# Kernel optimization log

Hardware: AMD Instinct MI355X
Metric: run time of the kernel (lower is better)

The kernel has to match this reference:

```python
import jax, jax.numpy as jnp
import numpy as np

D = 128      # state_dim
ED = 20      # edge_dim (RBF basis size)
R = 3        # num message/update rounds
G = 3        # gated equivariant blocks
CUT = 5.0    # cutoff
N = 10000    # nodes
E = 160000   # edges
B = 500      # molecules
HRO = 64     # readout hidden


def setup_inputs() -> dict:
    key = jax.random.key(0)
    ks = jax.random.split(key, 40)
    sc = 0.05

    def nrm(k, shape):
        return jax.random.normal(k, shape, dtype=jnp.float32) * sc

    inp = {
        "h": jax.random.normal(ks[0], (N, 5), dtype=jnp.float32),
        "pos": jax.random.normal(ks[1], (N, 3), dtype=jnp.float32),
        "edge_index": jax.random.randint(ks[2], (2, E), 0, N),
        "batch": jnp.sort(jax.random.randint(ks[3], (N,), 0, B)),
        # node embedding Linear(5, D)
        "emb_w": nrm(ks[4], (5, D)), "emb_b": nrm(ks[5], (D,)),
        # per-round message params (stacked over rounds)
        "msg_phi_w1": nrm(ks[6], (R, D, D)), "msg_phi_b1": nrm(ks[7], (R, D)),
        "msg_phi_w2": nrm(ks[8], (R, D, 3 * D)), "msg_phi_b2": nrm(ks[9], (R, 3 * D)),
        "msg_filt_w": nrm(ks[10], (R, ED, 3 * D)), "msg_filt_b": nrm(ks[11], (R, 3 * D)),
        # per-round update params
        "upd_U": nrm(ks[12], (R, D, D)), "upd_V": nrm(ks[13], (R, D, D)),
        "upd_w1": nrm(ks[14], (R, 2 * D, D)), "upd_b1": nrm(ks[15], (R, D)),
        "upd_w2": nrm(ks[16], (R, D, 3 * D)), "upd_b2": nrm(ks[17], (R, 3 * D)),
        # gated equivariant blocks
        "geb_wv1": nrm(ks[18], (G, D, D)), "geb_wv2": nrm(ks[19], (G, D, D)),
        "geb_w1": nrm(ks[20], (G, 2 * D, D)), "geb_b1": nrm(ks[21], (G, D)),
        "geb_w2": nrm(ks[22], (G, D, 2 * D)), "geb_b2": nrm(ks[23], (G, 2 * D)),
        # invariant readout MLP
        "ro_w1": nrm(ks[24], (D, HRO)), "ro_b1": nrm(ks[25], (HRO,)),
        "ro_w2": nrm(ks[26], (HRO, 1)), "ro_b2": nrm(ks[27], (1,)),
    }
    return inp


def _safe_norm(x, axis):
    return jnp.sqrt(jnp.sum(x * x, axis=axis) + 1e-8)


def reference(h, pos, edge_index, batch,
              emb_w, emb_b,
              msg_phi_w1, msg_phi_b1, msg_phi_w2, msg_phi_b2,
              msg_filt_w, msg_filt_b,
              upd_U, upd_V, upd_w1, upd_b1, upd_w2, upd_b2,
              geb_wv1, geb_wv2, geb_w1, geb_b1, geb_w2, geb_b2,
              ro_w1, ro_b1, ro_w2, ro_b2):
    n_nodes = h.shape[0]
    row, col = edge_index[0], edge_index[1]
    # edge vectors: r_ij = pos[col] - pos[row]
    r_ij = pos[col] - pos[row]                                   # [E,3]
    d = jnp.clip(jnp.linalg.norm(r_ij, axis=1, keepdims=True), 1e-6, None)  # [E,1]
    unit = r_ij / d                                              # [E,3]
    # sinc radial basis + cosine cutoff
    freqs = jnp.arange(1, ED + 1, dtype=h.dtype)
    rbf = jnp.sin(freqs * jnp.pi * d / CUT) / d                  # [E,ED]
    fcut = 0.5 * (jnp.cos(jnp.pi * d / CUT) + 1.0) * (d < CUT)   # [E,1]

    s = h @ emb_w + emb_b                                        # [N,D]
    v = jnp.zeros((n_nodes, D, 3), dtype=h.dtype)                # [N,D,3]

    for r in range(R):
        # --- PaiNNMessage ---
        phi = jax.nn.silu(s @ msg_phi_w1[r] + msg_phi_b1[r]) @ msg_phi_w2[r] + msg_phi_b2[r]  # [N,3D]
        filt = (rbf @ msg_filt_w[r] + msg_filt_b[r]) * fcut      # [E,3D]
        x = phi[col] * filt                                      # gather + modulate  [E,3D]
        xs, xvv, xvw = jnp.split(x, 3, axis=-1)                  # each [E,D]
        ds = jax.ops.segment_sum(xs, row, num_segments=n_nodes)  # [N,D]
        dv_e = xvv[:, :, None] * v[col] + xvw[:, :, None] * unit[:, None, :]  # [E,D,3]
        dv = jax.ops.segment_sum(dv_e, row, num_segments=n_nodes)             # [N,D,3]
        s = s + ds
        v = v + dv
        # --- PaiNNUpdate ---
        Uv = jnp.einsum('ndc,de->nec', v, upd_U[r])              # [N,D,3]
        Vv = jnp.einsum('ndc,de->nec', v, upd_V[r])              # [N,D,3]
        Vn = _safe_norm(Vv, axis=-1)                             # [N,D]
        a = jax.nn.silu(jnp.concatenate([s, Vn], axis=-1) @ upd_w1[r] + upd_b1[r]) @ upd_w2[r] + upd_b2[r]
        a_ss, a_sv, a_vv = jnp.split(a, 3, axis=-1)
        s = s + a_ss + a_sv * jnp.sum(Uv * Vv, axis=-1)
        v = v + a_vv[:, :, None] * Uv

    # --- GatedEquivariantBlocks ---
    for g in range(G):
        v1 = jnp.einsum('ndc,de->nec', v, geb_wv1[g])
        v2 = jnp.einsum('ndc,de->nec', v, geb_wv2[g])
        n2 = _safe_norm(v2, axis=-1)                             # [N,D]
        a = jax.nn.silu(jnp.concatenate([s, n2], axis=-1) @ geb_w1[g] + geb_b1[g]) @ geb_w2[g] + geb_b2[g]
        s_new, gate = jnp.split(a, 2, axis=-1)
        s = s_new
        v = gate[:, :, None] * v1

    # --- InvariantReadout + molwise scatter ---
    out = jax.nn.silu(s @ ro_w1 + ro_b1) @ ro_w2 + ro_b2         # [N,1]
    molwise = jax.ops.segment_sum(out, batch, num_segments=B)    # [B,1]
    return molwise.squeeze(-1)
```

## Files before the change

### kernel.cpp

```cpp
#include <hip/hip_runtime.h>

typedef __attribute__((ext_vector_type(4))) float f32x4;
typedef __attribute__((ext_vector_type(8))) short short8;

#define D 128
#define D3 384
#define SLD 256
#define EDIM 20
#define NR 3
#define NG 3
#define CUTOFF 5.0f
#define NNODES 10000
#define NEDGES 160000
#define NMOL 500
#define HROH 64
#define PI_F 3.14159265358979323846f

#define FBIAS 1
#define FSILU 2
#define FBF16O 4

static __device__ __forceinline__ float silu_f(float x) {
    return x / (1.0f + expf(-x));
}

static __device__ __forceinline__ ushort f2bf(float x) {
    uint u = __float_as_uint(x);
    uint r = (u + 0x7fffu + ((u >> 16) & 1u)) >> 16;
    return (ushort)r;
}
static __device__ __forceinline__ float bf2f(ushort h) {
    return __uint_as_float((uint)h << 16);
}

#define TLR 64
#define TLC 64
#define KC 32
#define APAD 40
#define BPAD 36

__global__ __launch_bounds__(256) void gemm_k(
    const float* __restrict__ A, int lda,
    const float* __restrict__ W, int ldw,
    const float* __restrict__ bias,
    float* __restrict__ C, ushort* __restrict__ Cbf, int ldc,
    int N, int K, int flags)
{
    const int n0 = blockIdx.x * TLR;
    const int m0 = blockIdx.y * TLC;
    __shared__ ushort Ah[TLR * APAD], Al[TLR * APAD];
    __shared__ ushort Bh[TLC * BPAD], Bl[TLC * BPAD];
    const int tid = threadIdx.x;
    const int arow = tid & 63;
    const int akq = (tid >> 6) * 4;
    const bool aok = (n0 + arow) < N;
    const float* Ar = A + (size_t)(n0 + arow) * lda;
    const int bk = tid >> 4;
    const int bm = (tid & 15) * 4;
    const float* Wp = W + m0 + bm;
    const int lane = tid & 63;
    const int wrow = (tid >> 6) * 16;
    const int fr = lane & 15;
    const int kg = lane >> 4;
    const ushort* aph = Ah + (wrow + fr) * APAD + kg * 8;
    const ushort* apl = Al + (wrow + fr) * APAD + kg * 8;

    f32x4 acc[4];
    #pragma unroll
    for (int t = 0; t < 4; ++t) acc[t] = (f32x4){0.f, 0.f, 0.f, 0.f};

    for (int k0 = 0; k0 < K; k0 += KC) {
        #pragma unroll
        for (int half = 0; half < 2; ++half) {
            int kk = akq + half * 16;
            float4 v = aok ? *(const float4*)(Ar + k0 + kk)
                           : make_float4(0.f, 0.f, 0.f, 0.f);
            ushort h0 = f2bf(v.x), h1 = f2bf(v.y), h2 = f2bf(v.z), h3 = f2bf(v.w);
            ushort l0 = f2bf(v.x - bf2f(h0)), l1 = f2bf(v.y - bf2f(h1));
            ushort l2 = f2bf(v.z - bf2f(h2)), l3 = f2bf(v.w - bf2f(h3));
            uint2 ph, pl;
            ph.x = (uint)h0 | ((uint)h1 << 16); ph.y = (uint)h2 | ((uint)h3 << 16);
            pl.x = (uint)l0 | ((uint)l1 << 16); pl.y = (uint)l2 | ((uint)l3 << 16);
            *(uint2*)(Ah + arow * APAD + kk) = ph;
            *(uint2*)(Al + arow * APAD + kk) = pl;
        }
        #pragma unroll
        for (int half = 0; half < 2; ++half) {
            int kk = bk + half * 16;
            float4 v = *(const float4*)(Wp + (size_t)(k0 + kk) * ldw);
            float vv[4] = {v.x, v.y, v.z, v.w};
            #pragma unroll
            for (int i = 0; i < 4; ++i) {
                ushort hh = f2bf(vv[i]);
                ushort ll = f2bf(vv[i] - bf2f(hh));
                Bh[(bm + i) * BPAD + kk] = hh;
                Bl[(bm + i) * BPAD + kk] = ll;
            }
        }
        __syncthreads();
        short8 ah = *(const short8*)aph;
        short8 al = *(const short8*)apl;
        #pragma unroll
        for (int t = 0; t < 4; ++t) {
            const ushort* bp = Bh + (t * 16 + fr) * BPAD + kg * 8;
            const ushort* bq = Bl + (t * 16 + fr) * BPAD + kg * 8;
            short8 bh, bl;
            ((uint2*)&bh)[0] = *(const uint2*)bp;
            ((uint2*)&bh)[1] = *(const uint2*)(bp + 4);
            ((uint2*)&bl)[0] = *(const uint2*)bq;
            ((uint2*)&bl)[1] = *(const uint2*)(bq + 4);
            acc[t] = __builtin_amdgcn_mfma_f32_16x16x32_bf16(ah, bh, acc[t], 0, 0, 0);
            acc[t] = __builtin_amdgcn_mfma_f32_16x16x32_bf16(al, bh, acc[t], 0, 0, 0);
            acc[t] = __builtin_amdgcn_mfma_f32_16x16x32_bf16(ah, bl, acc[t], 0, 0, 0);
        }
        __syncthreads();
    }
    #pragma unroll
    for (int t = 0; t < 4; ++t) {
        #pragma unroll
        for (int r = 0; r < 4; ++r) {
            int n = n0 + wrow + kg * 4 + r;
            if (n < N) {
                int m = m0 + t * 16 + fr;
                float val = acc[t][r];
                if (flags & FBIAS) val += bias[m];
                if (flags & FSILU) val = silu_f(val);
                if (flags & FBF16O) Cbf[(size_t)n * ldc + m] = f2bf(val);
                else                C[(size_t)n * ldc + m] = val;
            }
        }
    }
}

template <bool WITHDOT>
__global__ __launch_bounds__(256) void uvn_k(
    const float* __restrict__ A,
    const float* __restrict__ WU, const float* __restrict__ WV,
    float* __restrict__ Uv,
    float* __restrict__ DOT,
    float* __restrict__ SX, int N)
{
    const int n0 = blockIdx.x * 64;
    const int m0 = blockIdx.y * 64;
    __shared__ ushort Ah[3][64 * APAD], Al[3][64 * APAD];
    __shared__ ushort Bh[2][64 * BPAD], Bl[2][64 * BPAD];
    const int tid = threadIdx.x;
    const int arow = tid & 63;
    const int akq = (tid >> 6) * 4;
    const bool aok = (n0 + arow) < N;
    const float* Ar = A + (size_t)(n0 + arow) * D3;
    const int bk = tid >> 4;
    const int bm = (tid & 15) * 4;
    const int lane = tid & 63;
    const int wrow = (tid >> 6) * 16;
    const int fr = lane & 15;
    const int kg = lane >> 4;

    f32x4 acc[3][2][4];
    #pragma unroll
    for (int c = 0; c < 3; ++c)
        #pragma unroll
        for (int s = 0; s < 2; ++s)
            #pragma unroll
            for (int t = 0; t < 4; ++t) acc[c][s][t] = (f32x4){0.f, 0.f, 0.f, 0.f};

    for (int k0 = 0; k0 < D; k0 += KC) {
        #pragma unroll
        for (int c = 0; c < 3; ++c) {
            #pragma unroll
            for (int half = 0; half < 2; ++half) {
                int kk = akq + half * 16;
                float4 v = aok ? *(const float4*)(Ar + c * D + k0 + kk)
                               : make_float4(0.f, 0.f, 0.f, 0.f);
                ushort h0 = f2bf(v.x), h1 = f2bf(v.y), h2 = f2bf(v.z), h3 = f2bf(v.w);
                ushort l0 = f2bf(v.x - bf2f(h0)), l1 = f2bf(v.y - bf2f(h1));
                ushort l2 = f2bf(v.z - bf2f(h2)), l3 = f2bf(v.w - bf2f(h3));
                uint2 ph, pl;
                ph.x = (uint)h0 | ((uint)h1 << 16); ph.y = (uint)h2 | ((uint)h3 << 16);
                pl.x = (uint)l0 | ((uint)l1 << 16); pl.y = (uint)l2 | ((uint)l3 << 16);
                *(uint2*)(&Ah[c][arow * APAD + kk]) = ph;
                *(uint2*)(&Al[c][arow * APAD + kk]) = pl;
            }
        }
        #pragma unroll
        for (int s = 0; s < 2; ++s) {
            const float* W = s ? WV : WU;
            #pragma unroll
            for (int half = 0; half < 2; ++half) {
                int kk = bk + half * 16;
                float4 v = *(const float4*)(W + (size_t)(k0 + kk) * D + m0 + bm);
                float vv[4] = {v.x, v.y, v.z, v.w};
                #pragma unroll
                for (int i = 0; i < 4; ++i) {
                    ushort hh = f2bf(vv[i]);
                    ushort ll = f2bf(vv[i] - bf2f(hh));
                    Bh[s][(bm + i) * BPAD + kk] = hh;
                    Bl[s][(bm + i) * BPAD + kk] = ll;
                }
            }
        }
        __syncthreads();
        short8 ah[3], al[3];
        #pragma unroll
        for (int c = 0; c < 3; ++c) {
            ah[c] = *(const short8*)(&Ah[c][(wrow + fr) * APAD + kg * 8]);
            al[c] = *(const short8*)(&Al[c][(wrow + fr) * APAD + kg * 8]);
        }
        #pragma unroll
        for (int t = 0; t < 4; ++t) {
            #pragma unroll
            for (int s = 0; s < 2; ++s) {
                const ushort* bp = &Bh[s][(t * 16 + fr) * BPAD + kg * 8];
                const ushort* bq = &Bl[s][(t * 16 + fr) * BPAD + kg * 8];
                short8 bh, bl;
                ((uint2*)&bh)[0] = *(const uint2*)bp;
                ((uint2*)&bh)[1] = *(const uint2*)(bp + 4);
                ((uint2*)&bl)[0] = *(const uint2*)bq;
                ((uint2*)&bl)[1] = *(const uint2*)(bq + 4);
                #pragma unroll
                for (int c = 0; c < 3; ++c) {
                    acc[c][s][t] = __builtin_amdgcn_mfma_f32_16x16x32_bf16(ah[c], bh, acc[c][s][t], 0, 0, 0);
                    acc[c][s][t] = __builtin_amdgcn_mfma_f32_16x16x32_bf16(al[c], bh, acc[c][s][t], 0, 0, 0);
                    acc[c][s][t] = __builtin_amdgcn_mfma_f32_16x16x32_bf16(ah[c], bl, acc[c][s][t], 0, 0, 0);
                }
            }
        }
        __syncthreads();
    }
    #pragma unroll
    for (int t = 0; t < 4; ++t) {
        #pragma unroll
        for (int r = 0; r < 4; ++r) {
            int n = n0 + wrow + kg * 4 + r;
            if (n < N) {
                int m = m0 + t * 16 + fr;
                float ux = acc[0][0][t][r], uy = acc[1][0][t][r], uz = acc[2][0][t][r];
                float vx = acc[0][1][t][r], vy = acc[1][1][t][r], vz = acc[2][1][t][r];
                float* up = Uv + (size_t)n * D3 + m;
                up[0]     = ux;
                up[D]     = uy;
                up[2 * D] = uz;
                SX[(size_t)n * SLD + D + m] =
                    sqrtf(fmaf(vx, vx, fmaf(vy, vy, fmaf(vz, vz, 1e-8f))));
                if (WITHDOT)
                    DOT[(size_t)n * D + m] = fmaf(ux, vx, fmaf(uy, vy, uz * vz));
            }
        }
    }
}

__global__ __launch_bounds__(256) void emb_k(
    const float* __restrict__ h, const float* __restrict__ w,
    const float* __restrict__ b, float* __restrict__ s, int total)
{
    int i = blockIdx.x * 256 + threadIdx.x;
    if (i >= total) return;
    int n = i >> 7, d = i & 127;
    float acc = b[d];
    #pragma unroll
    for (int k = 0; k < 5; ++k) acc = fmaf(h[n * 5 + k], w[k * D + d], acc);
    s[(size_t)n * SLD + d] = acc;
}

__global__ __launch_bounds__(256) void hist_k(const int* __restrict__ ei,
                                              int* __restrict__ cnt, int E)
{
    int e = blockIdx.x * 256 + threadIdx.x;
    if (e < E) atomicAdd(&cnt[ei[e]], 1);
}

__global__ __launch_bounds__(256) void scan_k(const int* __restrict__ cnt,
                                              int* __restrict__ offs, int n)
{
    __shared__ int tmp[256];
    __shared__ int carry;
    if (threadIdx.x == 0) carry = 0;
    __syncthreads();
    for (int base = 0; base < n; base += 256) {
        int i = base + threadIdx.x;
        int v = (i < n) ? cnt[i] : 0;
        tmp[threadIdx.x] = v;
        __syncthreads();
        for (int off = 1; off < 256; off <<= 1) {
            int add = (threadIdx.x >= off) ? tmp[threadIdx.x - off] : 0;
            __syncthreads();
            tmp[threadIdx.x] += add;
            __syncthreads();
        }
        if (i < n) offs[i + 1] = carry + tmp[threadIdx.x];
        __syncthreads();
        if (threadIdx.x == 255) carry += tmp[255];
        __syncthreads();
    }
    if (threadIdx.x == 0) offs[0] = 0;
}

__global__ __launch_bounds__(256) void initnext_k(const int* __restrict__ offs,
                                                  int* __restrict__ next, int n)
{
    int i = blockIdx.x * 256 + threadIdx.x;
    if (i < n) next[i] = offs[i];
}

__global__ __launch_bounds__(256) void edge_pre_k(
    const int* __restrict__ ei, const float* __restrict__ pos,
    int* __restrict__ next, float* __restrict__ rbf_s,
    float* __restrict__ uf_s, int* __restrict__ col_s, int E)
{
    int e = blockIdx.x * 256 + threadIdx.x;
    if (e >= E) return;
    int r = ei[e], c = ei[E + e];
    float dx = pos[c * 3 + 0] - pos[r * 3 + 0];
    float dy = pos[c * 3 + 1] - pos[r * 3 + 1];
    float dz = pos[c * 3 + 2] - pos[r * 3 + 2];
    float dist = sqrtf(dx * dx + dy * dy + dz * dz);
    float d = fmaxf(dist, 1e-6f);
    float inv = 1.0f / d;
    int p = atomicAdd(&next[r], 1);
    col_s[p] = c;
    uf_s[p * 4 + 0] = dx * inv;
    uf_s[p * 4 + 1] = dy * inv;
    uf_s[p * 4 + 2] = dz * inv;
    uf_s[p * 4 + 3] = (d < CUTOFF) ? 0.5f * (cosf(PI_F * d / CUTOFF) + 1.0f) : 0.0f;
    float w = PI_F * d / CUTOFF;
    #pragma unroll
    for (int k = 1; k <= EDIM; ++k)
        rbf_s[(size_t)p * EDIM + (k - 1)] = sinf((float)k * w) * inv;
}

#define MSG_NPB 4
__global__ __launch_bounds__(256) void message_csr_k(
    const int* __restrict__ offs, const int* __restrict__ col_s,
    const float* __restrict__ rbf_s, const float* __restrict__ uf_s,
    const ushort* __restrict__ Pbf, const float* __restrict__ Vold,
    const ushort* __restrict__ VbfOld,
    const float* __restrict__ Wf, const float* __restrict__ bf,
    float* __restrict__ S, float* __restrict__ Vnew,
    ushort* __restrict__ VbfNew, int N)
{
    const int sub = threadIdx.x >> 7;
    const int d = threadIdx.x & 127;
    float ws[EDIM], wvv[EDIM], wvw[EDIM];
    #pragma unroll
    for (int k = 0; k < EDIM; ++k) {
        ws[k]  = Wf[k * D3 + d];
        wvv[k] = Wf[k * D3 + D + d];
        wvw[k] = Wf[k * D3 + 2 * D + d];
    }
    const float bs = bf[d], bvv = bf[D + d], bvw = bf[2 * D + d];

    auto edge = [&](int j, float& ds, float& dvx, float& dvy, float& dvz) {
        float4 u4 = *(const float4*)(uf_s + (size_t)j * 4);
        int col = col_s[j];
        const float* rb = rbf_s + (size_t)j * EDIM;
        float4 r0 = *(const float4*)(rb);
        float4 r1 = *(const float4*)(rb + 4);
        float4 r2 = *(const float4*)(rb + 8);
        float4 r3 = *(const float4*)(rb + 12);
        float4 r4 = *(const float4*)(rb + 16);
        float rv[EDIM] = {r0.x, r0.y, r0.z, r0.w, r1.x, r1.y, r1.z, r1.w,
                          r2.x, r2.y, r2.z, r2.w, r3.x, r3.y, r3.z, r3.w,
                          r4.x, r4.y, r4.z, r4.w};
        float fs = bs, fvv = bvv, fvw = bvw;
        #pragma unroll
        for (int k = 0; k < EDIM; ++k) {
            fs  = fmaf(rv[k], ws[k], fs);
            fvv = fmaf(rv[k], wvv[k], fvv);
            fvw = fmaf(rv[k], wvw[k], fvw);
        }
        float fc = u4.w;
        const ushort* pc = Pbf + (size_t)col * D3;
        const ushort* vc = VbfOld + (size_t)col * D3;
        float xs  = bf2f(pc[d]) * fs * fc;
        float xvv = bf2f(pc[D + d]) * fvv * fc;
        float xvw = bf2f(pc[2 * D + d]) * fvw * fc;
        ds += xs;
        dvx = fmaf(xvv, bf2f(vc[d]),         fmaf(xvw, u4.x, dvx));
        dvy = fmaf(xvv, bf2f(vc[D + d]),     fmaf(xvw, u4.y, dvy));
        dvz = fmaf(xvv, bf2f(vc[2 * D + d]), fmaf(xvw, u4.z, dvz));
    };

    for (int it = 0; it < MSG_NPB / 2; ++it) {
        int n = blockIdx.x * MSG_NPB + it * 2 + sub;
        if (n >= N) return;
        float ds0 = 0.f, dx0 = 0.f, dy0 = 0.f, dz0 = 0.f;
        float ds1 = 0.f, dx1 = 0.f, dy1 = 0.f, dz1 = 0.f;
        const int j0 = offs[n], j1 = offs[n + 1];
        int j = j0;
        for (; j + 2 <= j1; j += 2) {
            edge(j, ds0, dx0, dy0, dz0);
            edge(j + 1, ds1, dx1, dy1, dz1);
        }
        if (j < j1) edge(j, ds0, dx0, dy0, dz0);
        S[(size_t)n * SLD + d] += ds0 + ds1;
        const float* vo = Vold + (size_t)n * D3;
        float* vn = Vnew + (size_t)n * D3;
        ushort* vb = VbfNew + (size_t)n * D3;
        float nx = vo[d] + dx0 + dx1;
        float ny = vo[D + d] + dy0 + dy1;
        float nz = vo[2 * D + d] + dz0 + dz1;
        vn[d] = nx;         vb[d] = f2bf(nx);
        vn[D + d] = ny;     vb[D + d] = f2bf(ny);
        vn[2 * D + d] = nz; vb[2 * D + d] = f2bf(nz);
    }
}

__global__ __launch_bounds__(256) void upd_apply_k(
    const float* __restrict__ U3, const float* __restrict__ DOT,
    const float* __restrict__ P, float* __restrict__ s,
    float* __restrict__ v, ushort* __restrict__ vbf, int total)
{
    int i = blockIdx.x * 256 + threadIdx.x;
    if (i >= total) return;
    int n = i >> 7, d = i & 127;
    const float* u = U3 + (size_t)n * D3;
    float ux = u[d], uy = u[D + d], uz = u[2 * D + d];
    const float* a = P + (size_t)n * D3;
    s[(size_t)n * SLD + d] += a[d] + a[D + d] * DOT[i];
    float avv = a[2 * D + d];
    float* vv = v + (size_t)n * D3;
    ushort* vb = vbf + (size_t)n * D3;
    float nx = fmaf(avv, ux, vv[d]);
    float ny = fmaf(avv, uy, vv[D + d]);
    float nz = fmaf(avv, uz, vv[2 * D + d]);
    vv[d] = nx;         vb[d] = f2bf(nx);
    vv[D + d] = ny;     vb[D + d] = f2bf(ny);
    vv[2 * D + d] = nz; vb[2 * D + d] = f2bf(nz);
}

__global__ __launch_bounds__(256) void geb_apply_k(
    const float* __restrict__ P, const float* __restrict__ U3,
    float* __restrict__ s, float* __restrict__ v, int total)
{
    int i = blockIdx.x * 256 + threadIdx.x;
    if (i >= total) return;
    int n = i >> 7, d = i & 127;
    const float* a = P + (size_t)n * 2 * D;
    s[(size_t)n * SLD + d] = a[d];
    float g = a[D + d];
    const float* u = U3 + (size_t)n * D3;
    float* vv = v + (size_t)n * D3;
    vv[d]         = g * u[d];
    vv[D + d]     = g * u[D + d];
    vv[2 * D + d] = g * u[2 * D + d];
}

__global__ __launch_bounds__(256) void readout_k(
    const float* __restrict__ H2, const float* __restrict__ w2,
    const float* __restrict__ b2, const int* __restrict__ batch,
    float* __restrict__ out, int N)
{
    int n = blockIdx.x * 256 + threadIdx.x;
    if (n >= N) return;
    float acc = b2[0];
    const float* hrow = H2 + (size_t)n * HROH;
    #pragma unroll
    for (int k = 0; k < HROH; ++k) acc = fmaf(hrow[k], w2[k], acc);
    atomicAdd(out + batch[n], acc);
}


static inline void gemm(hipStream_t st, const float* A, int lda,
                        const float* W, int ldw, const float* bias,
                        float* C, ushort* Cbf, int ldc,
                        int N, int K, int M, int flags)
{
    dim3 g((N + TLR - 1) / TLR, M / TLC, 1);
    hipLaunchKernelGGL(gemm_k, g, dim3(256), 0, st,
                       A, lda, W, ldw, bias, C, Cbf, ldc, N, K, flags);
}

extern "C" void kernel_launch(void* const* d_in, const int* in_sizes, int n_in,
                              void* d_out, int out_size, void* d_ws, size_t ws_size,
                              hipStream_t stream)
{
    const float* h          = (const float*)d_in[0];
    const float* pos        = (const float*)d_in[1];
    const int*   ei         = (const int*)d_in[2];
    const int*   batch      = (const int*)d_in[3];
    const float* emb_w      = (const float*)d_in[4];
    const float* emb_b      = (const float*)d_in[5];
    const float* msg_phi_w1 = (const float*)d_in[6];
    const float* msg_phi_b1 = (const float*)d_in[7];
    const float* msg_phi_w2 = (const float*)d_in[8];
    const float* msg_phi_b2 = (const float*)d_in[9];
    const float* msg_filt_w = (const float*)d_in[10];
    const float* msg_filt_b = (const float*)d_in[11];
    const float* upd_U      = (const float*)d_in[12];
    const float* upd_V      = (const float*)d_in[13];
    const float* upd_w1     = (const float*)d_in[14];
    const float* upd_b1     = (const float*)d_in[15];
    const float* upd_w2     = (const float*)d_in[16];
    const float* upd_b2     = (const float*)d_in[17];
    const float* geb_wv1    = (const float*)d_in[18];
    const float* geb_wv2    = (const float*)d_in[19];
    const float* geb_w1     = (const float*)d_in[20];
    const float* geb_b1     = (const float*)d_in[21];
    const float* geb_w2     = (const float*)d_in[22];
    const float* geb_b2     = (const float*)d_in[23];
    const float* ro_w1      = (const float*)d_in[24];
    const float* ro_b1      = (const float*)d_in[25];
    const float* ro_w2      = (const float*)d_in[26];
    const float* ro_b2      = (const float*)d_in[27];
    float* out = (float*)d_out;

    const int N = NNODES, E = NEDGES;

    char* p = (char*)d_ws;
    auto carve = [&](size_t bytes) {
        char* r = p;
        p += (bytes + 255) & ~(size_t)255;
        return r;
    };
    float*  SX   = (float*)carve((size_t)N * SLD * 4);
    float*  VA   = (float*)carve((size_t)N * D3 * 4);
    float*  VB   = (float*)carve((size_t)N * D3 * 4);
    float*  P_   = (float*)carve((size_t)N * D3 * 4);
    ushort* Pbf  = (ushort*)P_;
    ushort* VBFa = (ushort*)carve((size_t)N * D3 * 2);
    ushort* VBFb = (ushort*)carve((size_t)N * D3 * 2);
    float*  H    = (float*)carve((size_t)N * D * 4);
    float*  H2   = (float*)carve((size_t)N * D * 4);
    float*  RBFs = (float*)carve((size_t)E * EDIM * 4);
    float*  UFs  = (float*)carve((size_t)E * 4 * 4);
    int*    COLs = (int*)carve((size_t)E * 4);
    int*    offs = (int*)carve((size_t)(N + 1) * 4);
    int*    nxt  = (int*)carve((size_t)N * 4);

    hipMemsetAsync(VA, 0, (size_t)N * D3 * 4, stream);
    hipMemsetAsync(VBFa, 0, (size_t)N * D3 * 2, stream);
    hipLaunchKernelGGL(emb_k, dim3((N * D + 255) / 256), dim3(256), 0, stream,
                       h, emb_w, emb_b, SX, N * D);
    hipMemsetAsync(nxt, 0, (size_t)N * 4, stream);
    hipLaunchKernelGGL(hist_k, dim3((E + 255) / 256), dim3(256), 0, stream, ei, nxt, E);
    hipLaunchKernelGGL(scan_k, dim3(1), dim3(256), 0, stream, nxt, offs, N);
    hipLaunchKernelGGL(initnext_k, dim3((N + 255) / 256), dim3(256), 0, stream,
                       offs, nxt, N);
    hipLaunchKernelGGL(edge_pre_k, dim3((E + 255) / 256), dim3(256), 0, stream,
                       ei, pos, nxt, RBFs, UFs, COLs, E);

    float*  Vc = VA;   ushort* VbfC = VBFa;
    float*  Vs = VB;   ushort* VbfS = VBFb;

    for (int r = 0; r < NR; ++r) {
        gemm(stream, SX, SLD, msg_phi_w1 + (size_t)r * D * D, D,
             msg_phi_b1 + (size_t)r * D, H, nullptr, D, N, D, D, FBIAS | FSILU);
        gemm(stream, H, D, msg_phi_w2 + (size_t)r * D * D3, D3,
             msg_phi_b2 + (size_t)r * D3, nullptr, Pbf, D3, N, D, D3,
             FBIAS | FBF16O);
        hipLaunchKernelGGL(message_csr_k, dim3((N + MSG_NPB - 1) / MSG_NPB),
                           dim3(256), 0, stream,
                           offs, COLs, RBFs, UFs, Pbf, Vc, VbfC,
                           msg_filt_w + (size_t)r * EDIM * D3,
                           msg_filt_b + (size_t)r * D3, SX, Vs, VbfS, N);
        { float* t = Vc; Vc = Vs; Vs = t; }
        { ushort* t = VbfC; VbfC = VbfS; VbfS = t; }
        float* Uv = Vs;
        hipLaunchKernelGGL(HIP_KERNEL_NAME(uvn_k<true>),
                           dim3((N + 63) / 64, 2), dim3(256), 0, stream,
                           Vc, upd_U + (size_t)r * D * D,
                           upd_V + (size_t)r * D * D, Uv, H, SX, N);
        gemm(stream, SX, SLD, upd_w1 + (size_t)r * 2 * D * D, D,
             upd_b1 + (size_t)r * D, H2, nullptr, D, N, 2 * D, D, FBIAS | FSILU);
        gemm(stream, H2, D, upd_w2 + (size_t)r * D * D3, D3,
             upd_b2 + (size_t)r * D3, P_, nullptr, D3, N, D, D3, FBIAS);
        hipLaunchKernelGGL(upd_apply_k, dim3((N * D + 255) / 256), dim3(256), 0,
                           stream, Uv, H, P_, SX, Vc, VbfC, N * D);
    }

    for (int g = 0; g < NG; ++g) {
        float* Uv = Vs;
        hipLaunchKernelGGL(HIP_KERNEL_NAME(uvn_k<false>),
                           dim3((N + 63) / 64, 2), dim3(256), 0, stream,
                           Vc, geb_wv1 + (size_t)g * D * D,
                           geb_wv2 + (size_t)g * D * D, Uv, nullptr, SX, N);
        gemm(stream, SX, SLD, geb_w1 + (size_t)g * 2 * D * D, D,
             geb_b1 + (size_t)g * D, H2, nullptr, D, N, 2 * D, D, FBIAS | FSILU);
        gemm(stream, H2, D, geb_w2 + (size_t)g * D * 2 * D, 2 * D,
             geb_b2 + (size_t)g * 2 * D, P_, nullptr, 2 * D, N, D, 2 * D, FBIAS);
        hipLaunchKernelGGL(geb_apply_k, dim3((N * D + 255) / 256), dim3(256), 0,
                           stream, P_, Uv, SX, Vc, N * D);
    }

    gemm(stream, SX, SLD, ro_w1, HROH, ro_b1, H2, nullptr, HROH, N, D, HROH,
         FBIAS | FSILU);
    hipMemsetAsync(out, 0, (size_t)NMOL * 4, stream);
    hipLaunchKernelGGL(readout_k, dim3((N + 255) / 256), dim3(256), 0, stream,
                       H2, ro_w2, ro_b2, batch, out, N);
}
```

Before: 936.4 us.

## Precompute edge filters with MFMA GEMM and shrink uvn tile rows

The per-edge RBF filter projection (20x384 FMAs per edge, done inline in the message kernel with weights held in registers) is moved into a separate padded-K GEMM on the MFMA path. The cutoff factor is fused into the GEMM epilogue and the result is stored as bf16 per edge, so the message kernel only loads three bf16 filter values per edge. This adds a write and read of an E x 384 bf16 buffer each round and lowers filter precision to bf16. Separately, uvn_k is retiled to 32 rows per block with waves split over column halves, doubling the grid size.

```diff
diff --git a/kernel.cpp b/kernel.cpp
--- a/kernel.cpp
+++ b/kernel.cpp
@@ -7,6 +7,7 @@
 #define D3 384
 #define SLD 256
 #define EDIM 20
+#define KPAD 32
 #define NR 3
 #define NG 3
 #define CUTOFF 5.0f
@@ -19,6 +20,7 @@
 #define FBIAS 1
 #define FSILU 2
 #define FBF16O 4
+#define FFCUT 8
 
 static __device__ __forceinline__ float silu_f(float x) {
     return x / (1.0f + expf(-x));
@@ -42,7 +44,7 @@
 __global__ __launch_bounds__(256) void gemm_k(
     const float* __restrict__ A, int lda,
     const float* __restrict__ W, int ldw,
-    const float* __restrict__ bias,
+    const float* __restrict__ bias, const float* __restrict__ fcut,
     float* __restrict__ C, ushort* __restrict__ Cbf, int ldc,
     int N, int K, int flags)
 {
@@ -124,6 +126,7 @@
                 int m = m0 + t * 16 + fr;
                 float val = acc[t][r];
                 if (flags & FBIAS) val += bias[m];
+                if (flags & FFCUT) val *= fcut[(size_t)n * 4];
                 if (flags & FSILU) val = silu_f(val);
                 if (flags & FBF16O) Cbf[(size_t)n * ldc + m] = f2bf(val);
                 else                C[(size_t)n * ldc + m] = val;
@@ -140,47 +143,45 @@
     float* __restrict__ DOT,
     float* __restrict__ SX, int N)
 {
-    const int n0 = blockIdx.x * 64;
+    const int n0 = blockIdx.x * 32;
     const int m0 = blockIdx.y * 64;
-    __shared__ ushort Ah[3][64 * APAD], Al[3][64 * APAD];
+    __shared__ ushort Ah[3][32 * APAD], Al[3][32 * APAD];
     __shared__ ushort Bh[2][64 * BPAD], Bl[2][64 * BPAD];
     const int tid = threadIdx.x;
-    const int arow = tid & 63;
-    const int akq = (tid >> 6) * 4;
+    const int arow = tid & 31;
+    const int akq = (tid >> 5) * 4;
     const bool aok = (n0 + arow) < N;
     const float* Ar = A + (size_t)(n0 + arow) * D3;
     const int bk = tid >> 4;
     const int bm = (tid & 15) * 4;
+    const int w = tid >> 6;
+    const int rt = w & 1;
+    const int ch = w >> 1;
     const int lane = tid & 63;
-    const int wrow = (tid >> 6) * 16;
     const int fr = lane & 15;
     const int kg = lane >> 4;
 
-    f32x4 acc[3][2][4];
+    f32x4 acc[3][2][2];
     #pragma unroll
     for (int c = 0; c < 3; ++c)
         #pragma unroll
         for (int s = 0; s < 2; ++s)
             #pragma unroll
-            for (int t = 0; t < 4; ++t) acc[c][s][t] = (f32x4){0.f, 0.f, 0.f, 0.f};
+            for (int t = 0; t < 2; ++t) acc[c][s][t] = (f32x4){0.f, 0.f, 0.f, 0.f};
 
     for (int k0 = 0; k0 < D; k0 += KC) {
         #pragma unroll
         for (int c = 0; c < 3; ++c) {
-            #pragma unroll
-            for (int half = 0; half < 2; ++half) {
-                int kk = akq + half * 16;
-                float4 v = aok ? *(const float4*)(Ar + c * D + k0 + kk)
-                               : make_float4(0.f, 0.f, 0.f, 0.f);
-                ushort h0 = f2bf(v.x), h1 = f2bf(v.y), h2 = f2bf(v.z), h3 = f2bf(v.w);
-                ushort l0 = f2bf(v.x - bf2f(h0)), l1 = f2bf(v.y - bf2f(h1));
-                ushort l2 = f2bf(v.z - bf2f(h2)), l3 = f2bf(v.w - bf2f(h3));
-                uint2 ph, pl;
-                ph.x = (uint)h0 | ((uint)h1 << 16); ph.y = (uint)h2 | ((uint)h3 << 16);
-                pl.x = (uint)l0 | ((uint)l1 << 16); pl.y = (uint)l2 | ((uint)l3 << 16);
-                *(uint2*)(&Ah[c][arow * APAD + kk]) = ph;
-                *(uint2*)(&Al[c][arow * APAD + kk]) = pl;
-            }
+            float4 v = aok ? *(const float4*)(Ar + c * D + k0 + akq)
+                           : make_float4(0.f, 0.f, 0.f, 0.f);
+            ushort h0 = f2bf(v.x), h1 = f2bf(v.y), h2 = f2bf(v.z), h3 = f2bf(v.w);
+            ushort l0 = f2bf(v.x - bf2f(h0)), l1 = f2bf(v.y - bf2f(h1));
+            ushort l2 = f2bf(v.z - bf2f(h2)), l3 = f2bf(v.w - bf2f(h3));
+            uint2 ph, pl;
+            ph.x = (uint)h0 | ((uint)h1 << 16); ph.y = (uint)h2 | ((uint)h3 << 16);
+            pl.x = (uint)l0 | ((uint)l1 << 16); pl.y = (uint)l2 | ((uint)l3 << 16);
+            *(uint2*)(&Ah[c][arow * APAD + akq]) = ph;
+            *(uint2*)(&Al[c][arow * APAD + akq]) = pl;
         }
         #pragma unroll
         for (int s = 0; s < 2; ++s) {
@@ -203,15 +204,15 @@
         short8 ah[3], al[3];
         #pragma unroll
         for (int c = 0; c < 3; ++c) {
-            ah[c] = *(const short8*)(&Ah[c][(wrow + fr) * APAD + kg * 8]);
-            al[c] = *(const short8*)(&Al[c][(wrow + fr) * APAD + kg * 8]);
-        }
-        #pragma unroll
-        for (int t = 0; t < 4; ++t) {
+            ah[c] = *(const short8*)(&Ah[c][(rt * 16 + fr) * APAD + kg * 8]);
+            al[c] = *(const short8*)(&Al[c][(rt * 16 + fr) * APAD + kg * 8]);
+        }
+        #pragma unroll
+        for (int t = 0; t < 2; ++t) {
             #pragma unroll
             for (int s = 0; s < 2; ++s) {
-                const ushort* bp = &Bh[s][(t * 16 + fr) * BPAD + kg * 8];
-                const ushort* bq = &Bl[s][(t * 16 + fr) * BPAD + kg * 8];
+                const ushort* bp = &Bh[s][(ch * 32 + t * 16 + fr) * BPAD + kg * 8];
+                const ushort* bq = &Bl[s][(ch * 32 + t * 16 + fr) * BPAD + kg * 8];
                 short8 bh, bl;
                 ((uint2*)&bh)[0] = *(const uint2*)bp;
                 ((uint2*)&bh)[1] = *(const uint2*)(bp + 4);
@@ -228,12 +229,12 @@
         __syncthreads();
     }
     #pragma unroll
-    for (int t = 0; t < 4; ++t) {
+    for (int t = 0; t < 2; ++t) {
         #pragma unroll
         for (int r = 0; r < 4; ++r) {
-            int n = n0 + wrow + kg * 4 + r;
+            int n = n0 + rt * 16 + kg * 4 + r;
             if (n < N) {
-                int m = m0 + t * 16 + fr;
+                int m = m0 + ch * 32 + t * 16 + fr;
                 float ux = acc[0][0][t][r], uy = acc[1][0][t][r], uz = acc[2][0][t][r];
                 float vx = acc[0][1][t][r], vy = acc[1][1][t][r], vz = acc[2][1][t][r];
                 float* up = Uv + (size_t)n * D3 + m;
@@ -260,6 +261,17 @@
     #pragma unroll
     for (int k = 0; k < 5; ++k) acc = fmaf(h[n * 5 + k], w[k * D + d], acc);
     s[(size_t)n * SLD + d] = acc;
+}
+
+__global__ __launch_bounds__(256) void wfpad_k(const float* __restrict__ w,
+                                               float* __restrict__ wp)
+{
+    int i = blockIdx.x * 256 + threadIdx.x;
+    if (i >= 3 * KPAD * D3) return;
+    int r = i / (KPAD * D3);
+    int rem = i % (KPAD * D3);
+    int k = rem / D3, m = rem % D3;
+    wp[i] = (k < EDIM) ? w[((size_t)r * EDIM + k) * D3 + m] : 0.f;
 }
 
 __global__ __launch_bounds__(256) void hist_k(const int* __restrict__ ei,
@@ -323,57 +335,38 @@
     uf_s[p * 4 + 2] = dz * inv;
     uf_s[p * 4 + 3] = (d < CUTOFF) ? 0.5f * (cosf(PI_F * d / CUTOFF) + 1.0f) : 0.0f;
     float w = PI_F * d / CUTOFF;
+    float* rb = rbf_s + (size_t)p * KPAD;
     #pragma unroll
     for (int k = 1; k <= EDIM; ++k)
-        rbf_s[(size_t)p * EDIM + (k - 1)] = sinf((float)k * w) * inv;
+        rb[k - 1] = sinf((float)k * w) * inv;
+    #pragma unroll
+    for (int k = EDIM; k < KPAD; ++k) rb[k] = 0.f;
 }
 
 #define MSG_NPB 4
 __global__ __launch_bounds__(256) void message_csr_k(
     const int* __restrict__ offs, const int* __restrict__ col_s,
-    const float* __restrict__ rbf_s, const float* __restrict__ uf_s,
+    const ushort* __restrict__ FILT, const float* __restrict__ uf_s,
     const ushort* __restrict__ Pbf, const float* __restrict__ Vold,
     const ushort* __restrict__ VbfOld,
-    const float* __restrict__ Wf, const float* __restrict__ bf,
     float* __restrict__ S, float* __restrict__ Vnew,
     ushort* __restrict__ VbfNew, int N)
 {
     const int sub = threadIdx.x >> 7;
     const int d = threadIdx.x & 127;
-    float ws[EDIM], wvv[EDIM], wvw[EDIM];
-    #pragma unroll
-    for (int k = 0; k < EDIM; ++k) {
-        ws[k]  = Wf[k * D3 + d];
-        wvv[k] = Wf[k * D3 + D + d];
-        wvw[k] = Wf[k * D3 + 2 * D + d];
-    }
-    const float bs = bf[d], bvv = bf[D + d], bvw = bf[2 * D + d];
 
     auto edge = [&](int j, float& ds, float& dvx, float& dvy, float& dvz) {
+        const ushort* fp = FILT + (size_t)j * D3;
+        float f0 = bf2f(fp[d]);
+        float f1 = bf2f(fp[D + d]);
+        float f2 = bf2f(fp[2 * D + d]);
+        int col = col_s[j];
         float4 u4 = *(const float4*)(uf_s + (size_t)j * 4);
-        int col = col_s[j];
-        const float* rb = rbf_s + (size_t)j * EDIM;
-        float4 r0 = *(const float4*)(rb);
-        float4 r1 = *(const float4*)(rb + 4);
-        float4 r2 = *(const float4*)(rb + 8);
-        float4 r3 = *(const float4*)(rb + 12);
-        float4 r4 = *(const float4*)(rb + 16);
-        float rv[EDIM] = {r0.x, r0.y, r0.z, r0.w, r1.x, r1.y, r1.z, r1.w,
-                          r2.x, r2.y, r2.z, r2.w, r3.x, r3.y, r3.z, r3.w,
-                          r4.x, r4.y, r4.z, r4.w};
-        float fs = bs, fvv = bvv, fvw = bvw;
-        #pragma unroll
-        for (int k = 0; k < EDIM; ++k) {
-            fs  = fmaf(rv[k], ws[k], fs);
-            fvv = fmaf(rv[k], wvv[k], fvv);
-            fvw = fmaf(rv[k], wvw[k], fvw);
-        }
-        float fc = u4.w;
         const ushort* pc = Pbf + (size_t)col * D3;
         const ushort* vc = VbfOld + (size_t)col * D3;
-        float xs  = bf2f(pc[d]) * fs * fc;
-        float xvv = bf2f(pc[D + d]) * fvv * fc;
-        float xvw = bf2f(pc[2 * D + d]) * fvw * fc;
+        float xs  = bf2f(pc[d]) * f0;
+        float xvv = bf2f(pc[D + d]) * f1;
+        float xvw = bf2f(pc[2 * D + d]) * f2;
         ds += xs;
         dvx = fmaf(xvv, bf2f(vc[d]),         fmaf(xvw, u4.x, dvx));
         dvy = fmaf(xvv, bf2f(vc[D + d]),     fmaf(xvw, u4.y, dvy));
@@ -462,12 +455,13 @@
 
 static inline void gemm(hipStream_t st, const float* A, int lda,
                         const float* W, int ldw, const float* bias,
+                        const float* fcut,
                         float* C, ushort* Cbf, int ldc,
                         int N, int K, int M, int flags)
 {
     dim3 g((N + TLR - 1) / TLR, M / TLC, 1);
     hipLaunchKernelGGL(gemm_k, g, dim3(256), 0, st,
-                       A, lda, W, ldw, bias, C, Cbf, ldc, N, K, flags);
+                       A, lda, W, ldw, bias, fcut, C, Cbf, ldc, N, K, flags);
 }
 
 extern "C" void kernel_launch(void* const* d_in, const int* in_sizes, int n_in,
@@ -521,49 +515,57 @@
     ushort* VBFb = (ushort*)carve((size_t)N * D3 * 2);
     float*  H    = (float*)carve((size_t)N * D * 4);
     float*  H2   = (float*)carve((size_t)N * D * 4);
-    float*  RBFs = (float*)carve((size_t)E * EDIM * 4);
+    float*  RBFp = (float*)carve((size_t)E * KPAD * 4);
     float*  UFs  = (float*)carve((size_t)E * 4 * 4);
     int*    COLs = (int*)carve((size_t)E * 4);
     int*    offs = (int*)carve((size_t)(N + 1) * 4);
     int*    nxt  = (int*)carve((size_t)N * 4);
+    float*  WFP  = (float*)carve((size_t)3 * KPAD * D3 * 4);
+    ushort* FILT = (ushort*)carve((size_t)E * D3 * 2);
 
     hipMemsetAsync(VA, 0, (size_t)N * D3 * 4, stream);
     hipMemsetAsync(VBFa, 0, (size_t)N * D3 * 2, stream);
     hipLaunchKernelGGL(emb_k, dim3((N * D + 255) / 256), dim3(256), 0, stream,
                        h, emb_w, emb_b, SX, N * D);
+    hipLaunchKernelGGL(wfpad_k, dim3((3 * KPAD * D3 + 255) / 256), dim3(256), 0,
+                       stream, msg_filt_w, WFP);
     hipMemsetAsync(nxt, 0, (size_t)N * 4, stream);
     hipLaunchKernelGGL(hist_k, dim3((E + 255) / 256), dim3(256), 0, stream, ei, nxt, E);
     hipLaunchKernelGGL(scan_k, dim3(1), dim3(256), 0, stream, nxt, offs, N);
     hipLaunchKernelGGL(initnext_k, dim3((N + 255) / 256), dim3(256), 0, stream,
                        offs, nxt, N);
     hipLaunchKernelGGL(edge_pre_k, dim3((E + 255) / 256), dim3(256), 0, stream,
-                       ei, pos, nxt, RBFs, UFs, COLs, E);
+                       ei, pos, nxt, RBFp, UFs, COLs, E);
 
     float*  Vc = VA;   ushort* VbfC = VBFa;
     float*  Vs = VB;   ushort* VbfS = VBFb;
 
     for (int r = 0; r < NR; ++r) {
+        gemm(stream, RBFp, KPAD, WFP + (size_t)r * KPAD * D3, D3,
+             msg_filt_b + (size_t)r * D3, UFs + 3, nullptr, FILT, D3,
+             E, KPAD, D3, FBIAS | FFCUT | FBF16O);
         gemm(stream, SX, SLD, msg_phi_w1 + (size_t)r * D * D, D,
-             msg_phi_b1 + (size_t)r * D, H, nullptr, D, N, D, D, FBIAS | FSILU);
+             msg_phi_b1 + (size_t)r * D, nullptr, H, nullptr, D, N, D, D,
+             FBIAS | FSILU);
         gemm(stream, H, D, msg_phi_w2 + (size_t)r * D * D3, D3,
-             msg_phi_b2 + (size_t)r * D3, nullptr, Pbf, D3, N, D, D3,
+             msg_phi_b2 + (size_t)r * D3, nullptr, nullptr, Pbf, D3, N, D, D3,
              FBIAS | FBF16O);
         hipLaunchKernelGGL(message_csr_k, dim3((N + MSG_NPB - 1) / MSG_NPB),
                            dim3(256), 0, stream,
-                           offs, COLs, RBFs, UFs, Pbf, Vc, VbfC,
-                           msg_filt_w + (size_t)r * EDIM * D3,
-                           msg_filt_b + (size_t)r * D3, SX, Vs, VbfS, N);
+                           offs, COLs, FILT, UFs, Pbf, Vc, VbfC,
+                           SX, Vs, VbfS, N);
         { float* t = Vc; Vc = Vs; Vs = t; }
         { ushort* t = VbfC; VbfC = VbfS; VbfS = t; }
         float* Uv = Vs;
         hipLaunchKernelGGL(HIP_KERNEL_NAME(uvn_k<true>),
-                           dim3((N + 63) / 64, 2), dim3(256), 0, stream,
+                           dim3((N + 31) / 32, 2), dim3(256), 0, stream,
                            Vc, upd_U + (size_t)r * D * D,
                            upd_V + (size_t)r * D * D, Uv, H, SX, N);
         gemm(stream, SX, SLD, upd_w1 + (size_t)r * 2 * D * D, D,
-             upd_b1 + (size_t)r * D, H2, nullptr, D, N, 2 * D, D, FBIAS | FSILU);
+             upd_b1 + (size_t)r * D, nullptr, H2, nullptr, D, N, 2 * D, D,
+             FBIAS | FSILU);
         gemm(stream, H2, D, upd_w2 + (size_t)r * D * D3, D3,
-             upd_b2 + (size_t)r * D3, P_, nullptr, D3, N, D, D3, FBIAS);
+             upd_b2 + (size_t)r * D3, nullptr, P_, nullptr, D3, N, D, D3, FBIAS);
         hipLaunchKernelGGL(upd_apply_k, dim3((N * D + 255) / 256), dim3(256), 0,
                            stream, Uv, H, P_, SX, Vc, VbfC, N * D);
     }
@@ -571,19 +573,21 @@
     for (int g = 0; g < NG; ++g) {
         float* Uv = Vs;
         hipLaunchKernelGGL(HIP_KERNEL_NAME(uvn_k<false>),
-                           dim3((N + 63) / 64, 2), dim3(256), 0, stream,
+                           dim3((N + 31) / 32, 2), dim3(256), 0, stream,
                            Vc, geb_wv1 + (size_t)g * D * D,
                            geb_wv2 + (size_t)g * D * D, Uv, nullptr, SX, N);
         gemm(stream, SX, SLD, geb_w1 + (size_t)g * 2 * D * D, D,
-             geb_b1 + (size_t)g * D, H2, nullptr, D, N, 2 * D, D, FBIAS | FSILU);
+             geb_b1 + (size_t)g * D, nullptr, H2, nullptr, D, N, 2 * D, D,
+             FBIAS | FSILU);
         gemm(stream, H2, D, geb_w2 + (size_t)g * D * 2 * D, 2 * D,
-             geb_b2 + (size_t)g * 2 * D, P_, nullptr, 2 * D, N, D, 2 * D, FBIAS);
+             geb_b2 + (size_t)g * 2 * D, nullptr, P_, nullptr, 2 * D, N, D, 2 * D,
+             FBIAS);
         hipLaunchKernelGGL(geb_apply_k, dim3((N * D + 255) / 256), dim3(256), 0,
                            stream, P_, Uv, SX, Vc, N * D);
     }
 
-    gemm(stream, SX, SLD, ro_w1, HROH, ro_b1, H2, nullptr, HROH, N, D, HROH,
-         FBIAS | FSILU);
+    gemm(stream, SX, SLD, ro_w1, HROH, ro_b1, nullptr, H2, nullptr, HROH,
+         N, D, HROH, FBIAS | FSILU);
     hipMemsetAsync(out, 0, (size_t)NMOL * 4, stream);
     hipLaunchKernelGGL(readout_k, dim3((N + 255) / 256), dim3(256), 0, stream,
                        H2, ro_w2, ro_b2, batch, out, N);
```

Result: slower. 1.045 ms (+11.6%).
